# Kernel optimization log

Measured on AMD Instinct MI355X. Metric: run time of the kernel, lower is better.

## Reference

```python
import jax, jax.numpy as jnp
import numpy as np

B, HI, WI, DIM = 16, 64, 64, 256
HEADS, HEAD_DIM, NUM_MEM = 8, 32, 4
HID = HEADS * HEAD_DIM


def setup_inputs() -> dict:
    key = jax.random.key(0)
    ks = jax.random.split(key, 6)
    return {
        "x": jax.random.normal(ks[0], (B, HI, WI, DIM), jnp.float32),
        "gamma_in": jax.random.normal(ks[1], (DIM,), jnp.float32) * 0.02,
        "w_qkv": jax.random.normal(ks[2], (DIM, 3 * HID), jnp.float32) / np.sqrt(DIM),
        "b_qkv": jnp.zeros((3 * HID,), jnp.float32),
        "mem_kv": jax.random.normal(ks[3], (2, HEADS, NUM_MEM, HEAD_DIM), jnp.float32),
        "w_out": jax.random.normal(ks[4], (HID, DIM), jnp.float32) / np.sqrt(HID),
        "b_out": jnp.zeros((DIM,), jnp.float32),
        "gamma_out": jax.random.normal(ks[5], (DIM,), jnp.float32) * 0.02,
    }


def reference(x, gamma_in, w_qkv, b_qkv, mem_kv, w_out, b_out, gamma_out):
    b, h, w, c = x.shape
    n = h * w
    rms_scale = c ** 0.5
    attn_scale = HEAD_DIM ** -0.5

    # RMSNorm (as written in source: pure learned scaling)
    xn = x * (gamma_in + 1.0) * rms_scale

    # 1x1 conv == per-pixel linear projection
    qkv = xn @ w_qkv + b_qkv                       # (b, h, w, 3*HID)
    q, k, v = jnp.split(qkv, 3, axis=-1)

    def to_heads(t):                                # (b,h,w,HID) -> (b, heads, d, n)
        return t.reshape(b, n, HEADS, HEAD_DIM).transpose(0, 2, 3, 1)

    q, k, v = map(to_heads, (q, k, v))

    # memory kv: (heads, m, d) -> (b, heads, d, m), concat along sequence axis
    mk = jnp.broadcast_to(mem_kv[0].transpose(0, 2, 1)[None], (b, HEADS, HEAD_DIM, NUM_MEM))
    mv = jnp.broadcast_to(mem_kv[1].transpose(0, 2, 1)[None], (b, HEADS, HEAD_DIM, NUM_MEM))
    k = jnp.concatenate([mk, k], axis=-1)           # (b, heads, d, n+m)
    v = jnp.concatenate([mv, v], axis=-1)

    # feature-map attention: softmax q over feature dim, k over sequence dim
    q = jax.nn.softmax(q * attn_scale, axis=-2)     # source scales q before softmax
    k = jax.nn.softmax(k, axis=-1)

    context = jnp.einsum('bhdn,bhen->bhde', k, v)   # (b, heads, d, e) small
    out = jnp.einsum('bhde,bhdn->bhen', context, q) # (b, heads, e, n)

    out = out.transpose(0, 3, 1, 2).reshape(b, h, w, HID)
    y = out @ w_out + b_out                         # 1x1 output conv
    return y * (gamma_out + 1.0) * rms_scale        # output RMSNorm
```

## Files before the change

kernel.cpp:

```cpp
#include <hip/hip_runtime.h>
#include <hip/hip_bf16.h>

typedef __bf16 bf16_t;
typedef _Float16 fp16_t;
typedef _Float16 f16x8 __attribute__((ext_vector_type(8)));
typedef _Float16 f16x4 __attribute__((ext_vector_type(4)));
typedef __bf16 bf16x4 __attribute__((ext_vector_type(4)));
typedef float f32x4 __attribute__((ext_vector_type(4)));

#define ATTN_SCALE 0.17677669529663687f
#define K_SHIFT 64.0f
#define Q_SHIFT 8.0f

__device__ __forceinline__ void gload16(const void* g, void* l) {
  __builtin_amdgcn_global_load_lds((const __attribute__((address_space(1))) void*)g,
                                   (__attribute__((address_space(3))) void*)l, 16, 0, 0);
}

__global__ __launch_bounds__(256) void prep_pack(
    const float* __restrict__ w_qkv, fp16_t* __restrict__ Bpack) {
  int idx = blockIdx.x * 256 + threadIdx.x;
  int l = idx & 63;
  int rest = idx >> 6;
  int f = rest & 3;
  int kk = (rest >> 2) & 7;
  int nt = rest >> 5;
  int n = nt * 64 + f * 16 + (l & 15);
  int k0 = kk * 32 + (l >> 4) * 8;
  f16x8 v;
#pragma unroll
  for (int e = 0; e < 8; ++e) v[e] = (fp16_t)w_qkv[(k0 + e) * 768 + n];
  ((f16x8*)Bpack)[idx] = v;
}

__global__ __launch_bounds__(256) void gemm_qvk_ctx(
    const float* __restrict__ x, const float* __restrict__ gamma_in,
    const fp16_t* __restrict__ Bpack, const float* __restrict__ bias,
    fp16_t* __restrict__ qe_out, float* __restrict__ part) {
  __shared__ fp16_t A[64 * 256];
  __shared__ bf16_t Pl[64 * 128];
  __shared__ fp16_t Vl[64 * 128];
  int t = threadIdx.x, l = t & 63, w = t >> 6;
  int lr = l >> 4, lc = l & 15;
  int bx = blockIdx.x;
  int m0 = bx * 64;

#pragma unroll
  for (int i = 0; i < 8; ++i) {
    int idx = i * 256 + t;
    int r = idx >> 5, c8 = idx & 31;
    const float* src = x + (size_t)(m0 + r) * 256 + c8 * 8;
    const float* gsc = gamma_in + c8 * 8;
    f16x8 hv;
#pragma unroll
    for (int j = 0; j < 8; ++j) hv[j] = (fp16_t)(src[j] * (gsc[j] + 1.f) * 16.f);
    *(f16x8*)&A[r * 256 + ((c8 ^ (r & 31)) * 8)] = hv;
  }
  __syncthreads();

  auto run_unit = [&](int nt, f32x4 acc[4][4]) {
    const fp16_t* Bp = Bpack + (size_t)nt * 16384;
#pragma unroll
    for (int mf = 0; mf < 4; ++mf)
#pragma unroll
      for (int nf = 0; nf < 4; ++nf) acc[mf][nf] = (f32x4){0.f, 0.f, 0.f, 0.f};
#pragma unroll
    for (int kk = 0; kk < 8; ++kk) {
      f16x8 af[4], bfr[4];
#pragma unroll
      for (int f = 0; f < 4; ++f) {
        int ra = f * 16 + lc;
        af[f] = *(const f16x8*)&A[ra * 256 + (((kk * 4 + lr) ^ (ra & 31)) * 8)];
        bfr[f] = *(const f16x8*)(Bp + (size_t)(kk * 4 + f) * 512 + l * 8);
      }
#pragma unroll
      for (int mf = 0; mf < 4; ++mf)
#pragma unroll
        for (int nf = 0; nf < 4; ++nf)
          acc[mf][nf] = __builtin_amdgcn_mfma_f32_16x16x32_f16(af[mf], bfr[nf], acc[mf][nf], 0, 0, 0);
    }
  };

  {
    f32x4 acc[4][4];
    run_unit(w, acc);
    int n0 = w * 64;
    float bq[4];
#pragma unroll
    for (int nf = 0; nf < 4; ++nf) bq[nf] = bias[n0 + nf * 16 + lc];
#pragma unroll
    for (int mf = 0; mf < 4; ++mf)
#pragma unroll
      for (int r = 0; r < 4; ++r) {
        int row = m0 + mf * 16 + lr * 4 + r;
#pragma unroll
        for (int nf = 0; nf < 4; ++nf) {
          float ql = (acc[mf][nf][r] + bq[nf]) * ATTN_SCALE;
          qe_out[(size_t)row * 256 + n0 + nf * 16 + lc] = (fp16_t)__expf(ql - Q_SHIFT);
        }
      }
  }

  int hq = t >> 6, s = t & 63;
  int d0 = (s >> 3) * 4, e0 = (s & 7) * 4;
  for (int ph = 0; ph < 2; ++ph) {
    f32x4 acc[4][4];
    int isK = (w < 2);
    int wu = isK ? w : (w - 2);
    int nt = (isK ? 4 : 8) + ph * 2 + wu;
    run_unit(nt, acc);
    int n0 = nt * 64;
    int lcb = wu * 64;
    float bv[4];
#pragma unroll
    for (int nf = 0; nf < 4; ++nf) bv[nf] = bias[n0 + nf * 16 + lc];
#pragma unroll
    for (int mf = 0; mf < 4; ++mf)
#pragma unroll
      for (int r = 0; r < 4; ++r) {
        int rl = mf * 16 + lr * 4 + r;
#pragma unroll
        for (int nf = 0; nf < 4; ++nf) {
          float val = acc[mf][nf][r] + bv[nf];
          if (isK) Pl[rl * 128 + lcb + nf * 16 + lc] = (bf16_t)__expf(val - K_SHIFT);
          else     Vl[rl * 128 + lcb + nf * 16 + lc] = (fp16_t)val;
        }
      }
    __syncthreads();

    float S[4][4] = {};
    float z[4] = {0.f, 0.f, 0.f, 0.f};
    int hb = hq * 32;
    for (int r = 0; r < 64; ++r) {
      bf16x4 pd4 = *(const bf16x4*)&Pl[r * 128 + hb + d0];
      f16x4 vv4 = *(const f16x4*)&Vl[r * 128 + hb + e0];
      float pd[4] = {(float)pd4[0], (float)pd4[1], (float)pd4[2], (float)pd4[3]};
      float vv[4] = {(float)vv4[0], (float)vv4[1], (float)vv4[2], (float)vv4[3]};
#pragma unroll
      for (int i = 0; i < 4; ++i) {
#pragma unroll
        for (int j = 0; j < 4; ++j) S[i][j] += pd[i] * vv[j];
        z[i] += pd[i];
      }
    }
    float* pp = part + (size_t)bx * 8448 + (ph * 4 + hq) * 1056;
#pragma unroll
    for (int i = 0; i < 4; ++i)
      *(float4*)&pp[(d0 + i) * 32 + e0] = (float4){S[i][0], S[i][1], S[i][2], S[i][3]};
    if (e0 == 0) {
#pragma unroll
      for (int i = 0; i < 4; ++i) pp[1024 + d0 + i] = z[i];
    }
    __syncthreads();
  }
}

__global__ __launch_bounds__(256) void build_wt(
    const float* __restrict__ part, const float* __restrict__ w_out,
    const float* __restrict__ mem_kv, fp16_t* __restrict__ Bpacky) {
  int bh = blockIdx.x;
  int b = bh >> 3, h = bh & 7;
  int t = threadIdx.x;
  __shared__ float S[32][32];
  __shared__ float Zr[32];
  __shared__ float W[32][256];
  for (int idx = t; idx < 1024; idx += 256) {
    float s = 0.f;
    for (int c = 0; c < 64; ++c) s += part[((size_t)(b * 64 + c)) * 8448 + h * 1056 + idx];
    S[idx >> 5][idx & 31] = s;
  }
  if (t < 32) {
    float zz = 0.f;
    for (int c = 0; c < 64; ++c) zz += part[((size_t)(b * 64 + c)) * 8448 + h * 1056 + 1024 + t];
    Zr[t] = zz;
  }
  for (int i = t; i < 32 * 256; i += 256) W[i >> 8][i & 255] = w_out[(h * 32 + (i >> 8)) * 256 + (i & 255)];
  __syncthreads();
  if (t < 32) {
    int dd = t;
    for (int m = 0; m < 4; ++m) {
      float p = __expf(mem_kv[h * 128 + m * 32 + dd] - K_SHIFT);
      Zr[dd] += p;
      for (int e = 0; e < 32; ++e) S[dd][e] += p * mem_kv[1024 + h * 128 + m * 32 + e];
    }
  }
  __syncthreads();
  int c = t;
  int nt = c >> 6, f = (c >> 4) & 3, lc = c & 15;
  for (int dd = 0; dd < 32; ++dd) {
    float acc = 0;
#pragma unroll 8
    for (int e = 0; e < 32; ++e) acc += S[dd][e] * W[e][c];
    int kcol = h * 32 + dd;
    int kk = kcol >> 5, lr = (kcol & 31) >> 3, e8 = kcol & 7;
    size_t addr = ((((size_t)(b * 4 + nt) * 8 + kk) * 4 + f) * 64 + (lr * 16 + lc)) * 8 + e8;
    Bpacky[addr] = (fp16_t)(acc / Zr[dd]);
  }
}

__global__ __launch_bounds__(256) void gemm_y(
    const fp16_t* __restrict__ qe, const fp16_t* __restrict__ Bpacky,
    const float* __restrict__ b_out, const float* __restrict__ gamma_out,
    float* __restrict__ y_out) {
  __shared__ fp16_t A[64 * 256];
  __shared__ float zbuf[64][8];
  int t = threadIdx.x, l = t & 63, w = t >> 6;
  int lr = l >> 4, lc = l & 15;
  int m0 = blockIdx.x * 64;
#pragma unroll
  for (int i = 0; i < 8; ++i) {
    int idx = i * 256 + t;
    int r = idx >> 5, cs = idx & 31;
    gload16(qe + (size_t)(m0 + r) * 256 + ((cs ^ (r & 31)) * 8), &A[idx * 8]);
  }
  __syncthreads();

#pragma unroll
  for (int pi = 0; pi < 2; ++pi) {
    int p = pi * 256 + t;
    int r = p >> 3, hh = p & 7;
    float zs = 0.f;
#pragma unroll
    for (int c = 0; c < 4; ++c) {
      int cs = (hh * 4 + c) ^ (r & 31);
      f16x8 vv = *(const f16x8*)&A[r * 256 + cs * 8];
#pragma unroll
      for (int j = 0; j < 8; ++j) zs += (float)vv[j];
    }
    zbuf[r][hh] = 1.f / zs;
  }
  __syncthreads();

#pragma unroll
  for (int i = 0; i < 8; ++i) {
    int idx = i * 256 + t;
    int r = idx >> 5, cs = idx & 31;
    int hh = (cs ^ (r & 31)) >> 2;
    float sc = zbuf[r][hh];
    f16x8 vv = *(const f16x8*)&A[idx * 8];
#pragma unroll
    for (int j = 0; j < 8; ++j) vv[j] = (fp16_t)((float)vv[j] * sc);
    *(f16x8*)&A[idx * 8] = vv;
  }
  __syncthreads();

  int n0 = w * 64;
  const fp16_t* Bp = Bpacky + (size_t)(m0 >> 12) * 65536 + (size_t)w * 16384;
  f32x4 acc[4][4];
#pragma unroll
  for (int mf = 0; mf < 4; ++mf)
#pragma unroll
    for (int nf = 0; nf < 4; ++nf) acc[mf][nf] = (f32x4){0.f, 0.f, 0.f, 0.f};
#pragma unroll
  for (int kk = 0; kk < 8; ++kk) {
    f16x8 af[4], bfr[4];
#pragma unroll
    for (int f = 0; f < 4; ++f) {
      int ra = f * 16 + lc;
      af[f] = *(const f16x8*)&A[ra * 256 + (((kk * 4 + lr) ^ (ra & 31)) * 8)];
      bfr[f] = *(const f16x8*)(Bp + (size_t)(kk * 4 + f) * 512 + l * 8);
    }
#pragma unroll
    for (int mf = 0; mf < 4; ++mf)
#pragma unroll
      for (int nf = 0; nf < 4; ++nf)
        acc[mf][nf] = __builtin_amdgcn_mfma_f32_16x16x32_f16(af[mf], bfr[nf], acc[mf][nf], 0, 0, 0);
  }
  float bv[4], gv[4];
#pragma unroll
  for (int nf = 0; nf < 4; ++nf) {
    int c = n0 + nf * 16 + lc;
    bv[nf] = b_out[c];
    gv[nf] = (gamma_out[c] + 1.f) * 16.f;
  }
#pragma unroll
  for (int mf = 0; mf < 4; ++mf)
#pragma unroll
    for (int r = 0; r < 4; ++r) {
      int row = m0 + mf * 16 + lr * 4 + r;
#pragma unroll
      for (int nf = 0; nf < 4; ++nf)
        y_out[(size_t)row * 256 + n0 + nf * 16 + lc] = (acc[mf][nf][r] + bv[nf]) * gv[nf];
    }
}

extern "C" void kernel_launch(void* const* d_in, const int* in_sizes, int n_in,
                              void* d_out, int out_size, void* d_ws, size_t ws_size,
                              hipStream_t stream) {
  const float* x        = (const float*)d_in[0];
  const float* gamma_in = (const float*)d_in[1];
  const float* w_qkv    = (const float*)d_in[2];
  const float* b_qkv    = (const float*)d_in[3];
  const float* mem_kv   = (const float*)d_in[4];
  const float* w_out    = (const float*)d_in[5];
  const float* b_out    = (const float*)d_in[6];
  const float* gamma_out= (const float*)d_in[7];
  float* y = (float*)d_out;

  char* ws = (char*)d_ws;
  fp16_t* qe     = (fp16_t*)(ws);
  fp16_t* Bpack  = (fp16_t*)(ws + 33554432);
  fp16_t* Bpacky = (fp16_t*)(ws + 33947648);
  float*  part   = (float*)(ws + 36044800);

  prep_pack<<<96, 256, 0, stream>>>(w_qkv, Bpack);
  gemm_qvk_ctx<<<1024, 256, 0, stream>>>(x, gamma_in, Bpack, b_qkv, qe, part);
  build_wt<<<128, 256, 0, stream>>>(part, w_out, mem_kv, Bpacky);
  gemm_y<<<1024, 256, 0, stream>>>(qe, Bpacky, b_out, gamma_out, y);
}
```

Before: 139.8 us.

## Compute per-tile K^T V context with MFMA instead of scalar FMA loops

The K/V projection is computed transposed (weights as the A operand, pixels as B), so exp(K) and V land in LDS feature-major with an XOR swizzle. The per-head context sum and the K normalizer are then computed with bf16 MFMA instructions, using a ones vector to produce the row sums, instead of a 64-iteration scalar FMA loop per thread. V is now stored as bf16 rather than fp16, which loses some precision. The K/V weights are packed into a separate buffer and the workspace layout is reshuffled to match.

```diff
diff --git a/kernel.cpp b/kernel.cpp
--- a/kernel.cpp
+++ b/kernel.cpp
@@ -4,8 +4,7 @@
 typedef __bf16 bf16_t;
 typedef _Float16 fp16_t;
 typedef _Float16 f16x8 __attribute__((ext_vector_type(8)));
-typedef _Float16 f16x4 __attribute__((ext_vector_type(4)));
-typedef __bf16 bf16x4 __attribute__((ext_vector_type(4)));
+typedef __bf16 bf16x8 __attribute__((ext_vector_type(8)));
 typedef float f32x4 __attribute__((ext_vector_type(4)));
 
 #define ATTN_SCALE 0.17677669529663687f
@@ -18,28 +17,37 @@
 }
 
 __global__ __launch_bounds__(256) void prep_pack(
-    const float* __restrict__ w_qkv, fp16_t* __restrict__ Bpack) {
+    const float* __restrict__ w_qkv, fp16_t* __restrict__ Bq, fp16_t* __restrict__ Akv) {
   int idx = blockIdx.x * 256 + threadIdx.x;
   int l = idx & 63;
-  int rest = idx >> 6;
-  int f = rest & 3;
-  int kk = (rest >> 2) & 7;
-  int nt = rest >> 5;
-  int n = nt * 64 + f * 16 + (l & 15);
-  int k0 = kk * 32 + (l >> 4) * 8;
-  f16x8 v;
-#pragma unroll
-  for (int e = 0; e < 8; ++e) v[e] = (fp16_t)w_qkv[(k0 + e) * 768 + n];
-  ((f16x8*)Bpack)[idx] = v;
+  if (idx < 8192) {
+    int f = (idx >> 6) & 3, kk = (idx >> 8) & 7, nt = idx >> 11;
+    int n = nt * 64 + f * 16 + (l & 15);
+    int k0 = kk * 32 + (l >> 4) * 8;
+    f16x8 v;
+#pragma unroll
+    for (int e = 0; e < 8; ++e) v[e] = (fp16_t)w_qkv[(k0 + e) * 768 + n];
+    ((f16x8*)Bq)[idx] = v;
+  } else {
+    int j = idx - 8192;
+    int f = (j >> 6) & 3, kk = (j >> 8) & 7, nt2 = j >> 11;
+    int col = 256 + nt2 * 64 + f * 16 + (l & 15);
+    int k0 = kk * 32 + (l >> 4) * 8;
+    f16x8 v;
+#pragma unroll
+    for (int e = 0; e < 8; ++e) v[e] = (fp16_t)w_qkv[(k0 + e) * 768 + col];
+    ((f16x8*)Akv)[j] = v;
+  }
 }
 
 __global__ __launch_bounds__(256) void gemm_qvk_ctx(
     const float* __restrict__ x, const float* __restrict__ gamma_in,
-    const fp16_t* __restrict__ Bpack, const float* __restrict__ bias,
+    const fp16_t* __restrict__ Bq, const fp16_t* __restrict__ Akv,
+    const float* __restrict__ bias,
     fp16_t* __restrict__ qe_out, float* __restrict__ part) {
   __shared__ fp16_t A[64 * 256];
-  __shared__ bf16_t Pl[64 * 128];
-  __shared__ fp16_t Vl[64 * 128];
+  __shared__ bf16_t Pl[128 * 64];
+  __shared__ bf16_t Vl[128 * 64];
   int t = threadIdx.x, l = t & 63, w = t >> 6;
   int lr = l >> 4, lc = l & 15;
   int bx = blockIdx.x;
@@ -58,8 +66,9 @@
   }
   __syncthreads();
 
-  auto run_unit = [&](int nt, f32x4 acc[4][4]) {
-    const fp16_t* Bp = Bpack + (size_t)nt * 16384;
+  {
+    const fp16_t* Bp = Bq + (size_t)w * 16384;
+    f32x4 acc[4][4];
 #pragma unroll
     for (int mf = 0; mf < 4; ++mf)
 #pragma unroll
@@ -79,11 +88,6 @@
         for (int nf = 0; nf < 4; ++nf)
           acc[mf][nf] = __builtin_amdgcn_mfma_f32_16x16x32_f16(af[mf], bfr[nf], acc[mf][nf], 0, 0, 0);
     }
-  };
-
-  {
-    f32x4 acc[4][4];
-    run_unit(w, acc);
     int n0 = w * 64;
     float bq[4];
 #pragma unroll
@@ -101,55 +105,90 @@
       }
   }
 
-  int hq = t >> 6, s = t & 63;
-  int d0 = (s >> 3) * 4, e0 = (s & 7) * 4;
+  bool isK = (w < 2);
+  int dl0 = (w & 1) * 64;
   for (int ph = 0; ph < 2; ++ph) {
+    int nt2 = (isK ? 0 : 4) + ph * 2 + (w & 1);
+    const fp16_t* Ap = Akv + (size_t)nt2 * 16384;
     f32x4 acc[4][4];
-    int isK = (w < 2);
-    int wu = isK ? w : (w - 2);
-    int nt = (isK ? 4 : 8) + ph * 2 + wu;
-    run_unit(nt, acc);
-    int n0 = nt * 64;
-    int lcb = wu * 64;
-    float bv[4];
-#pragma unroll
-    for (int nf = 0; nf < 4; ++nf) bv[nf] = bias[n0 + nf * 16 + lc];
+#pragma unroll
+    for (int mf = 0; mf < 4; ++mf)
+#pragma unroll
+      for (int nf = 0; nf < 4; ++nf) acc[mf][nf] = (f32x4){0.f, 0.f, 0.f, 0.f};
+#pragma unroll
+    for (int kk = 0; kk < 8; ++kk) {
+      f16x8 aw[4], bxn[4];
+#pragma unroll
+      for (int f = 0; f < 4; ++f) {
+        aw[f] = *(const f16x8*)(Ap + (size_t)(kk * 4 + f) * 512 + l * 8);
+        int rn = f * 16 + lc;
+        bxn[f] = *(const f16x8*)&A[rn * 256 + (((kk * 4 + lr) ^ (rn & 31)) * 8)];
+      }
+#pragma unroll
+      for (int mf = 0; mf < 4; ++mf)
+#pragma unroll
+        for (int nf = 0; nf < 4; ++nf)
+          acc[mf][nf] = __builtin_amdgcn_mfma_f32_16x16x32_f16(aw[mf], bxn[nf], acc[mf][nf], 0, 0, 0);
+    }
+    int bb = (isK ? 256 : 512) + ph * 128;
 #pragma unroll
     for (int mf = 0; mf < 4; ++mf)
 #pragma unroll
       for (int r = 0; r < 4; ++r) {
-        int rl = mf * 16 + lr * 4 + r;
+        int dl = dl0 + mf * 16 + lr * 4 + r;
+        float bvv = bias[bb + dl];
 #pragma unroll
         for (int nf = 0; nf < 4; ++nf) {
-          float val = acc[mf][nf][r] + bv[nf];
-          if (isK) Pl[rl * 128 + lcb + nf * 16 + lc] = (bf16_t)__expf(val - K_SHIFT);
-          else     Vl[rl * 128 + lcb + nf * 16 + lc] = (fp16_t)val;
+          float val = acc[mf][nf][r] + bvv;
+          int n = nf * 16 + lc;
+          int addr = dl * 64 + ((((n >> 3) ^ (dl & 7)) << 3) | (n & 7));
+          if (isK) Pl[addr] = (bf16_t)__expf(val - K_SHIFT);
+          else     Vl[addr] = (bf16_t)val;
         }
       }
     __syncthreads();
 
-    float S[4][4] = {};
-    float z[4] = {0.f, 0.f, 0.f, 0.f};
-    int hb = hq * 32;
-    for (int r = 0; r < 64; ++r) {
-      bf16x4 pd4 = *(const bf16x4*)&Pl[r * 128 + hb + d0];
-      f16x4 vv4 = *(const f16x4*)&Vl[r * 128 + hb + e0];
-      float pd[4] = {(float)pd4[0], (float)pd4[1], (float)pd4[2], (float)pd4[3]};
-      float vv[4] = {(float)vv4[0], (float)vv4[1], (float)vv4[2], (float)vv4[3]};
-#pragma unroll
-      for (int i = 0; i < 4; ++i) {
-#pragma unroll
-        for (int j = 0; j < 4; ++j) S[i][j] += pd[i] * vv[j];
-        z[i] += pd[i];
-      }
-    }
-    float* pp = part + (size_t)bx * 8448 + (ph * 4 + hq) * 1056;
-#pragma unroll
-    for (int i = 0; i < 4; ++i)
-      *(float4*)&pp[(d0 + i) * 32 + e0] = (float4){S[i][0], S[i][1], S[i][2], S[i][3]};
-    if (e0 == 0) {
-#pragma unroll
-      for (int i = 0; i < 4; ++i) pp[1024 + d0 + i] = z[i];
+    {
+      int hb = w * 32;
+      f32x4 sacc[2][2];
+      f32x4 zacc[2];
+#pragma unroll
+      for (int mf = 0; mf < 2; ++mf) {
+#pragma unroll
+        for (int nf = 0; nf < 2; ++nf) sacc[mf][nf] = (f32x4){0.f, 0.f, 0.f, 0.f};
+        zacc[mf] = (f32x4){0.f, 0.f, 0.f, 0.f};
+      }
+      bf16x8 ones;
+#pragma unroll
+      for (int i = 0; i < 8; ++i) ones[i] = (bf16_t)1.0f;
+#pragma unroll
+      for (int k2 = 0; k2 < 2; ++k2) {
+        bf16x8 ap[2], bv2[2];
+#pragma unroll
+        for (int mf = 0; mf < 2; ++mf) {
+          int dl = hb + mf * 16 + (l & 15);
+          ap[mf] = *(const bf16x8*)&Pl[dl * 64 + (((k2 * 4 + lr) ^ (dl & 7)) << 3)];
+          int el = hb + mf * 16 + (l & 15);
+          bv2[mf] = *(const bf16x8*)&Vl[el * 64 + (((k2 * 4 + lr) ^ (el & 7)) << 3)];
+        }
+#pragma unroll
+        for (int mf = 0; mf < 2; ++mf) {
+#pragma unroll
+          for (int nf = 0; nf < 2; ++nf)
+            sacc[mf][nf] = __builtin_amdgcn_mfma_f32_16x16x32_bf16(ap[mf], bv2[nf], sacc[mf][nf], 0, 0, 0);
+          zacc[mf] = __builtin_amdgcn_mfma_f32_16x16x32_bf16(ap[mf], ones, zacc[mf], 0, 0, 0);
+        }
+      }
+      float* pp = part + (size_t)bx * 8448 + (ph * 4 + w) * 1056;
+#pragma unroll
+      for (int mf = 0; mf < 2; ++mf)
+#pragma unroll
+        for (int r = 0; r < 4; ++r) {
+          int dd = mf * 16 + lr * 4 + r;
+#pragma unroll
+          for (int nf = 0; nf < 2; ++nf) pp[dd * 32 + nf * 16 + lc] = sacc[mf][nf][r];
+          if (lc == 0) pp[1024 + dd] = zacc[mf][r];
+        }
     }
     __syncthreads();
   }
@@ -299,12 +338,13 @@
 
   char* ws = (char*)d_ws;
   fp16_t* qe     = (fp16_t*)(ws);
-  fp16_t* Bpack  = (fp16_t*)(ws + 33554432);
-  fp16_t* Bpacky = (fp16_t*)(ws + 33947648);
-  float*  part   = (float*)(ws + 36044800);
-
-  prep_pack<<<96, 256, 0, stream>>>(w_qkv, Bpack);
-  gemm_qvk_ctx<<<1024, 256, 0, stream>>>(x, gamma_in, Bpack, b_qkv, qe, part);
+  fp16_t* Bq     = (fp16_t*)(ws + 33554432);
+  fp16_t* Akv    = (fp16_t*)(ws + 33685504);
+  float*  part   = (float*)(ws + 33947648);
+  fp16_t* Bpacky = (fp16_t*)(ws + 68550656);
+
+  prep_pack<<<96, 256, 0, stream>>>(w_qkv, Bq, Akv);
+  gemm_qvk_ctx<<<1024, 256, 0, stream>>>(x, gamma_in, Bq, Akv, b_qkv, qe, part);
   build_wt<<<128, 256, 0, stream>>>(part, w_out, mem_kv, Bpacky);
   gemm_y<<<1024, 256, 0, stream>>>(qe, Bpacky, b_out, gamma_out, y);
 }
```

After: 168.7 us. 1.21x slower.
